# Optimization experiments

Measured on AMD Instinct MI355X. Metric: run time of the kernel, lower is better.

The kernel has to match this reference:

```python
import jax, jax.numpy as jnp
import numpy as np

C_Z, H, C = 128, 4, 32
L = 320
SCALE = 1.0 / np.sqrt(C)
EPS = 1e-5


def setup_inputs() -> dict:
    key = jax.random.key(0)
    ks = jax.random.split(key, 8)
    s = 0.02
    return {
        "z": jax.random.normal(ks[0], (L, L, C_Z), dtype=jnp.float32),
        "pair_mask": jnp.ones((L, L), dtype=jnp.float32),
        "res_mask": jnp.ones((L,), dtype=bool),
        "ln_gamma": jnp.ones((C_Z,), dtype=jnp.float32),
        "ln_beta": jnp.zeros((C_Z,), dtype=jnp.float32),
        "Wq": jax.random.normal(ks[1], (C_Z, H * C), dtype=jnp.float32) * s,
        "Wk": jax.random.normal(ks[2], (C_Z, H * C), dtype=jnp.float32) * s,
        "Wv": jax.random.normal(ks[3], (C_Z, H * C), dtype=jnp.float32) * s,
        "Wb": jax.random.normal(ks[4], (C_Z, H), dtype=jnp.float32) * s,
        "Wg": jax.random.normal(ks[5], (C_Z, H * C), dtype=jnp.float32) * s,
        "Wout": jax.random.normal(ks[6], (H * C, C_Z), dtype=jnp.float32) * s,
    }


def _layernorm(x, gamma, beta):
    mu = jnp.mean(x, axis=-1, keepdims=True)
    var = jnp.mean(jnp.square(x - mu), axis=-1, keepdims=True)
    return (x - mu) * jax.lax.rsqrt(var + EPS) * gamma + beta


def reference(z, pair_mask, res_mask, ln_gamma, ln_beta, Wq, Wk, Wv, Wb, Wg, Wout):
    Ldim = z.shape[0]
    z_ln = _layernorm(z, ln_gamma, ln_beta)                      # [L,L,c_z]
    Q = (z_ln @ Wq).reshape(Ldim, Ldim, H, C)                    # [i,j,h,c]
    K = (z_ln @ Wk).reshape(Ldim, Ldim, H, C)                    # [i,k,h,c]
    V = (z_ln @ Wv).reshape(Ldim, Ldim, H, C)                    # [i,k,h,c]
    B = z_ln @ Wb                                                # [j,k,h]
    G = jax.nn.sigmoid(z_ln @ Wg).reshape(Ldim, Ldim, H, C)      # [i,j,h,c]

    # logits[i,h,j,k] = <Q[i,j], K[i,k]> * scale + B[j,k,h]
    logits = jnp.einsum("ijhc,ikhc->ihjk", Q, K) * SCALE
    logits = logits + jnp.transpose(B, (2, 0, 1))[None]          # +[1,h,j,k]
    neg_inf = jnp.asarray(-jnp.inf, logits.dtype)
    logits = jnp.where(res_mask[None, None, None, :], logits, neg_inf)
    attn = jax.nn.softmax(logits, axis=-1)                       # over k

    out = jnp.einsum("ihjk,ikhc->ijhc", attn, V)                 # [i,j,h,c]
    out = (G * out).reshape(Ldim, Ldim, H * C)
    dz = out @ Wout                                              # [L,L,c_z]
    return dz * pair_mask[..., None]
```

## Files before the change

kernel.cpp:

```cpp
#include <hip/hip_runtime.h>

#define LDIM 320
#define CZ 128
#define NH 4
#define CH 32
#define SCALE2F (0.17677669529663687f * 1.4426950408889634f)
#define LOG2E 1.4426950408889634f
#define LN_EPS 1e-5f

typedef __attribute__((ext_vector_type(8))) short bf16x8;
typedef __attribute__((ext_vector_type(4))) float f32x4;

__device__ __forceinline__ unsigned int pack_bf2(float a, float b) {
  unsigned int ua = __float_as_uint(a);
  unsigned int ub = __float_as_uint(b);
  unsigned int ra = (ua + 0x7fffu + ((ua >> 16) & 1u)) >> 16;
  unsigned int rb = (ub + 0x7fffu + ((ub >> 16) & 1u)) >> 16;
  return (ra & 0xffffu) | (rb << 16);
}

__device__ __forceinline__ unsigned short f2bf(float a) {
  unsigned int ua = __float_as_uint(a);
  return (unsigned short)((ua + 0x7fffu + ((ua >> 16) & 1u)) >> 16);
}

__device__ __forceinline__ float bf2f(unsigned short u) {
  return __uint_as_float(((unsigned int)u) << 16);
}

__global__ __launch_bounds__(256) void k_prep(
    const float* __restrict__ Wq, const float* __restrict__ Wk,
    const float* __restrict__ Wv, const float* __restrict__ Wb,
    const float* __restrict__ Wg, const float* __restrict__ Wout,
    unsigned short* __restrict__ Wt, unsigned short* __restrict__ Woutt)
{
  __shared__ __attribute__((aligned(16))) unsigned short buf[64 * 136];
  const int t = threadIdx.x, bid = blockIdx.x;
  const bool isOut = (bid >= 9);
  const int n0 = isOut ? (bid - 9) * 64 : bid * 64;
  const int nl = t & 63;
  const int n = n0 + nl;
#pragma unroll 8
  for (int it = 0; it < 32; ++it) {
    const int k = (t >> 6) + 4 * it;
    float v;
    if (isOut)        v = Wout[k * 128 + n];
    else if (n < 128) v = Wq[k * 128 + n];
    else if (n < 256) v = Wk[k * 128 + n - 128];
    else if (n < 384) v = Wv[k * 128 + n - 256];
    else if (n < 512) v = Wg[k * 128 + n - 384];
    else if (n < 516) v = Wb[k * 4 + n - 512];
    else              v = 0.f;
    buf[nl * 136 + k] = f2bf(v);
  }
  __syncthreads();
  unsigned short* dst = isOut ? Woutt : Wt;
#pragma unroll
  for (int it = 0; it < 4; ++it) {
    const int idx = t + 256 * it;
    const int rr = idx >> 4, ck = idx & 15;
    const uint4 d = *(const uint4*)&buf[rr * 136 + ck * 8];
    *(uint4*)(dst + (size_t)(n0 + rr) * 128 + ck * 8) = d;
  }
}

__global__ __launch_bounds__(256) void k_lnproj(
    const float* __restrict__ z, const float* __restrict__ gamma,
    const float* __restrict__ beta, const unsigned short* __restrict__ Wt,
    const int* __restrict__ rmask,
    unsigned short* __restrict__ Qg, unsigned short* __restrict__ Kg,
    unsigned short* __restrict__ Vg, unsigned short* __restrict__ Gg,
    float* __restrict__ Bh)
{
  __shared__ __attribute__((aligned(16))) unsigned short As[128 * 136];
  const int t = threadIdx.x;
  const int m0 = blockIdx.x * 128;
  const int rlane = t & 7;

  const float* gp = gamma + rlane * 16;
  const float* bp = beta + rlane * 16;
  const float4 g0 = *(const float4*)(gp + 0);
  const float4 g1 = *(const float4*)(gp + 4);
  const float4 g2 = *(const float4*)(gp + 8);
  const float4 g3 = *(const float4*)(gp + 12);
  const float4 b0 = *(const float4*)(bp + 0);
  const float4 b1 = *(const float4*)(bp + 4);
  const float4 b2 = *(const float4*)(bp + 8);
  const float4 b3 = *(const float4*)(bp + 12);

#pragma unroll
  for (int rr = 0; rr < 4; ++rr) {
    const int row = rr * 32 + (t >> 3);
    const float* zp = z + (size_t)(m0 + row) * CZ + rlane * 16;
    const float4 x0 = *(const float4*)(zp + 0);
    const float4 x1 = *(const float4*)(zp + 4);
    const float4 x2 = *(const float4*)(zp + 8);
    const float4 x3 = *(const float4*)(zp + 12);
    float s  = x0.x + x0.y + x0.z + x0.w + x1.x + x1.y + x1.z + x1.w +
               x2.x + x2.y + x2.z + x2.w + x3.x + x3.y + x3.z + x3.w;
    float ss = x0.x*x0.x + x0.y*x0.y + x0.z*x0.z + x0.w*x0.w +
               x1.x*x1.x + x1.y*x1.y + x1.z*x1.z + x1.w*x1.w +
               x2.x*x2.x + x2.y*x2.y + x2.z*x2.z + x2.w*x2.w +
               x3.x*x3.x + x3.y*x3.y + x3.z*x3.z + x3.w*x3.w;
    s  += __shfl_xor(s, 1);  ss += __shfl_xor(ss, 1);
    s  += __shfl_xor(s, 2);  ss += __shfl_xor(ss, 2);
    s  += __shfl_xor(s, 4);  ss += __shfl_xor(ss, 4);
    const float mu  = s * (1.f / 128.f);
    const float var = ss * (1.f / 128.f) - mu * mu;
    const float rs  = rsqrtf(var + LN_EPS);
    uint4 u0, u1;
    u0.x = pack_bf2((x0.x - mu) * rs * g0.x + b0.x, (x0.y - mu) * rs * g0.y + b0.y);
    u0.y = pack_bf2((x0.z - mu) * rs * g0.z + b0.z, (x0.w - mu) * rs * g0.w + b0.w);
    u0.z = pack_bf2((x1.x - mu) * rs * g1.x + b1.x, (x1.y - mu) * rs * g1.y + b1.y);
    u0.w = pack_bf2((x1.z - mu) * rs * g1.z + b1.z, (x1.w - mu) * rs * g1.w + b1.w);
    u1.x = pack_bf2((x2.x - mu) * rs * g2.x + b2.x, (x2.y - mu) * rs * g2.y + b2.y);
    u1.y = pack_bf2((x2.z - mu) * rs * g2.z + b2.z, (x2.w - mu) * rs * g2.w + b2.w);
    u1.z = pack_bf2((x3.x - mu) * rs * g3.x + b3.x, (x3.y - mu) * rs * g3.y + b3.y);
    u1.w = pack_bf2((x3.z - mu) * rs * g3.z + b3.z, (x3.w - mu) * rs * g3.w + b3.w);
    unsigned short* dst = &As[row * 136 + rlane * 16];
    *(uint4*)(dst + 0) = u0;
    *(uint4*)(dst + 8) = u1;
  }
  __syncthreads();

  const int w = t >> 6, lane = t & 63;
  const int m16 = lane & 15, qd = lane >> 4;
  const f32x4 z4 = {0.f, 0.f, 0.f, 0.f};

  bf16x8 af[2][4];
#pragma unroll
  for (int ks = 0; ks < 4; ++ks) {
    af[0][ks] = *(const bf16x8*)&As[(w * 32 + m16) * 136 + ks * 32 + qd * 8];
    af[1][ks] = *(const bf16x8*)&As[(w * 32 + 16 + m16) * 136 + ks * 32 + qd * 8];
  }

  for (int ntile = 0; ntile < 8; ++ntile) {
    f32x4 acc[2][4];
#pragma unroll
    for (int sub = 0; sub < 2; ++sub)
#pragma unroll
      for (int nt = 0; nt < 4; ++nt) acc[sub][nt] = z4;
#pragma unroll
    for (int ks = 0; ks < 4; ++ks) {
#pragma unroll
      for (int nt = 0; nt < 4; ++nt) {
        const bf16x8 bf = *(const bf16x8*)(
            Wt + (size_t)(ntile * 64 + nt * 16 + m16) * 128 + ks * 32 + qd * 8);
        acc[0][nt] = __builtin_amdgcn_mfma_f32_16x16x32_bf16(af[0][ks], bf, acc[0][nt], 0, 0, 0);
        acc[1][nt] = __builtin_amdgcn_mfma_f32_16x16x32_bf16(af[1][ks], bf, acc[1][nt], 0, 0, 0);
      }
    }
#pragma unroll
    for (int sub = 0; sub < 2; ++sub) {
#pragma unroll
      for (int r = 0; r < 4; ++r) {
        const int p = m0 + w * 32 + sub * 16 + qd * 4 + r;
        const int a = p / 320, bb = p - a * 320;
#pragma unroll
        for (int nt = 0; nt < 4; ++nt) {
          const int n = ntile * 64 + nt * 16 + m16;
          const int off = n & 127, hh = off >> 5, cc = off & 31;
          float val = acc[sub][nt][r];
          if (ntile >= 6) val = 1.f / (1.f + __expf(-val));
          unsigned short* dst =
              (ntile < 2 ? Qg : (ntile < 4 ? Kg : (ntile < 6 ? Vg : Gg)));
          dst[((size_t)(a * 4 + hh) * 320 + bb) * 32 + cc] = f2bf(val);
        }
      }
    }
  }

  {
    f32x4 acc0 = z4, acc1 = z4;
#pragma unroll
    for (int ks = 0; ks < 4; ++ks) {
      const bf16x8 bf = *(const bf16x8*)(
          Wt + (size_t)(512 + m16) * 128 + ks * 32 + qd * 8);
      acc0 = __builtin_amdgcn_mfma_f32_16x16x32_bf16(af[0][ks], bf, acc0, 0, 0, 0);
      acc1 = __builtin_amdgcn_mfma_f32_16x16x32_bf16(af[1][ks], bf, acc1, 0, 0, 0);
    }
    if (m16 < 4) {
#pragma unroll
      for (int r = 0; r < 4; ++r) {
        const int p0 = m0 + w * 32 + qd * 4 + r;
        const int p1 = p0 + 16;
        const float mk0 = rmask[p0 % 320] ? 0.f : -INFINITY;
        const float mk1 = rmask[p1 % 320] ? 0.f : -INFINITY;
        Bh[(size_t)m16 * 102400 + p0] = acc0[r] * LOG2E + mk0;
        Bh[(size_t)m16 * 102400 + p1] = acc1[r] * LOG2E + mk1;
      }
    }
  }
}

__global__ __launch_bounds__(256) void k_attn(
    const unsigned short* __restrict__ Qg, const unsigned short* __restrict__ Kg,
    const unsigned short* __restrict__ Vg, const unsigned short* __restrict__ Gg,
    const float* __restrict__ Bh, unsigned short* __restrict__ Obg)
{
  __shared__ __attribute__((aligned(16))) unsigned short Vt[32 * 328];
  __shared__ __attribute__((aligned(16))) unsigned short Ps[4][16 * 168];
  const int h = blockIdx.x, i = blockIdx.y;
  const int t = threadIdx.x;
  const size_t base = (size_t)(i * NH + h) * (LDIM * CH);

  {
    const int k0 = t >> 3, c4 = (t & 7) * 4;
#pragma unroll
    for (int it = 0; it < 10; ++it) {
      const int k = k0 + 32 * it;
      const uint2 d = *(const uint2*)(Vg + base + k * 32 + c4);
      Vt[(c4 + 0) * 328 + k] = (unsigned short)(d.x & 0xffffu);
      Vt[(c4 + 1) * 328 + k] = (unsigned short)(d.x >> 16);
      Vt[(c4 + 2) * 328 + k] = (unsigned short)(d.y & 0xffffu);
      Vt[(c4 + 3) * 328 + k] = (unsigned short)(d.y >> 16);
    }
  }
  __syncthreads();

  const int w = t >> 6, lane = t & 63;
  const int m16 = lane & 15, qd = lane >> 4;
  const f32x4 z4 = {0.f, 0.f, 0.f, 0.f};

  for (int jt = w; jt < 20; jt += 4) {
    const bf16x8 qfrag =
        *(const bf16x8*)(Qg + base + (size_t)(jt * 16 + m16) * 32 + qd * 8);

    f32x4 acc[20];
    __builtin_amdgcn_s_setprio(1);
#pragma unroll
    for (int kt = 0; kt < 20; ++kt) {
      const bf16x8 kf =
          *(const bf16x8*)(Kg + base + (size_t)(kt * 16 + m16) * 32 + qd * 8);
      acc[kt] = __builtin_amdgcn_mfma_f32_16x16x32_bf16(qfrag, kf, z4, 0, 0, 0);
    }
    __builtin_amdgcn_s_setprio(0);

    const float* bp = Bh + (size_t)h * 102400 +
                      (size_t)(jt * 16 + qd * 4) * 320 + m16;
    float mx[4] = {-INFINITY, -INFINITY, -INFINITY, -INFINITY};
#pragma unroll
    for (int kt = 0; kt < 20; ++kt) {
#pragma unroll
      for (int r = 0; r < 4; ++r) {
        const float s = fmaf(acc[kt][r], SCALE2F, bp[r * 320 + kt * 16]);
        acc[kt][r] = s;
        mx[r] = fmaxf(mx[r], s);
      }
    }
#pragma unroll
    for (int r = 0; r < 4; ++r) {
      mx[r] = fmaxf(mx[r], __shfl_xor(mx[r], 1));
      mx[r] = fmaxf(mx[r], __shfl_xor(mx[r], 2));
      mx[r] = fmaxf(mx[r], __shfl_xor(mx[r], 4));
      mx[r] = fmaxf(mx[r], __shfl_xor(mx[r], 8));
    }
    float l[4] = {0.f, 0.f, 0.f, 0.f};
#pragma unroll
    for (int kt = 0; kt < 20; ++kt) {
#pragma unroll
      for (int r = 0; r < 4; ++r) {
        const float p = __builtin_amdgcn_exp2f(acc[kt][r] - mx[r]);
        acc[kt][r] = p;
        l[r] += p;
      }
    }
#pragma unroll
    for (int r = 0; r < 4; ++r) {
      l[r] += __shfl_xor(l[r], 1);
      l[r] += __shfl_xor(l[r], 2);
      l[r] += __shfl_xor(l[r], 4);
      l[r] += __shfl_xor(l[r], 8);
    }
    float rl[4];
#pragma unroll
    for (int r = 0; r < 4; ++r) rl[r] = __builtin_amdgcn_rcpf(l[r]);

    f32x4 accO0 = z4, accO1 = z4;
#pragma unroll
    for (int hh = 0; hh < 2; ++hh) {
#pragma unroll
      for (int kt2 = 0; kt2 < 10; ++kt2) {
        const int kt = hh * 10 + kt2;
#pragma unroll
        for (int r = 0; r < 4; ++r)
          Ps[w][(qd * 4 + r) * 168 + kt2 * 16 + m16] = f2bf(acc[kt][r]);
      }
      __builtin_amdgcn_s_setprio(1);
#pragma unroll
      for (int ks = 0; ks < 5; ++ks) {
        const bf16x8 pf = *(const bf16x8*)&Ps[w][m16 * 168 + ks * 32 + qd * 8];
        const bf16x8 v0 =
            *(const bf16x8*)&Vt[m16 * 328 + hh * 160 + ks * 32 + qd * 8];
        const bf16x8 v1 =
            *(const bf16x8*)&Vt[(16 + m16) * 328 + hh * 160 + ks * 32 + qd * 8];
        accO0 = __builtin_amdgcn_mfma_f32_16x16x32_bf16(pf, v0, accO0, 0, 0, 0);
        accO1 = __builtin_amdgcn_mfma_f32_16x16x32_bf16(pf, v1, accO1, 0, 0, 0);
      }
      __builtin_amdgcn_s_setprio(0);
    }

#pragma unroll
    for (int r = 0; r < 4; ++r) {
      const int j = jt * 16 + qd * 4 + r;
      const float g0 = bf2f(Gg[base + (size_t)j * 32 + m16]);
      const float g1 = bf2f(Gg[base + (size_t)j * 32 + 16 + m16]);
      unsigned short* op = Obg + (size_t)(i * 320 + j) * 128 + h * 32;
      op[m16]      = f2bf(g0 * rl[r] * accO0[r]);
      op[16 + m16] = f2bf(g1 * rl[r] * accO1[r]);
    }
  }
}

__global__ __launch_bounds__(256) void k_out(
    const unsigned short* __restrict__ Obg, const unsigned short* __restrict__ Woutt,
    const float* __restrict__ pm, float* __restrict__ out)
{
  __shared__ __attribute__((aligned(16))) unsigned short As[128 * 136];
  __shared__ __attribute__((aligned(16))) unsigned short Bs[64 * 136];
  const int t = threadIdx.x;
  const int ntile = blockIdx.x;
  const int m0 = blockIdx.y * 128;

#pragma unroll
  for (int it = 0; it < 8; ++it) {
    const int idx = t + 256 * it;
    const int rr = idx >> 4, ck = idx & 15;
    const uint4 d = *(const uint4*)(Obg + (size_t)(m0 + rr) * 128 + ck * 8);
    *(uint4*)&As[rr * 136 + ck * 8] = d;
  }
  {
    const unsigned short* wrow = Woutt + (size_t)ntile * 64 * 128;
#pragma unroll
    for (int it = 0; it < 4; ++it) {
      const int idx = t + 256 * it;
      const int n = idx >> 4, ck = idx & 15;
      const uint4 d = *(const uint4*)(wrow + n * 128 + ck * 8);
      *(uint4*)&Bs[n * 136 + ck * 8] = d;
    }
  }
  __syncthreads();

  const int w = t >> 6, lane = t & 63;
  const int m16 = lane & 15, qd = lane >> 4;
  const f32x4 z4 = {0.f, 0.f, 0.f, 0.f};
  f32x4 acc[2][4];
#pragma unroll
  for (int sub = 0; sub < 2; ++sub)
#pragma unroll
    for (int nt = 0; nt < 4; ++nt) acc[sub][nt] = z4;

#pragma unroll
  for (int ks = 0; ks < 4; ++ks) {
    const bf16x8 af0 = *(const bf16x8*)&As[(w * 32 + m16) * 136 + qd * 8 + ks * 32];
    const bf16x8 af1 = *(const bf16x8*)&As[(w * 32 + 16 + m16) * 136 + qd * 8 + ks * 32];
#pragma unroll
    for (int nt = 0; nt < 4; ++nt) {
      const bf16x8 bf = *(const bf16x8*)&Bs[(nt * 16 + m16) * 136 + qd * 8 + ks * 32];
      acc[0][nt] = __builtin_amdgcn_mfma_f32_16x16x32_bf16(af0, bf, acc[0][nt], 0, 0, 0);
      acc[1][nt] = __builtin_amdgcn_mfma_f32_16x16x32_bf16(af1, bf, acc[1][nt], 0, 0, 0);
    }
  }

#pragma unroll
  for (int sub = 0; sub < 2; ++sub) {
#pragma unroll
    for (int r = 0; r < 4; ++r) {
      const int p = m0 + w * 32 + sub * 16 + qd * 4 + r;
      const float m = pm[p];
      float* orow = out + (size_t)p * 128 + ntile * 64;
#pragma unroll
      for (int nt = 0; nt < 4; ++nt)
        orow[nt * 16 + m16] = acc[sub][nt][r] * m;
    }
  }
}

extern "C" void kernel_launch(void* const* d_in, const int* in_sizes, int n_in,
                              void* d_out, int out_size, void* d_ws, size_t ws_size,
                              hipStream_t stream)
{
  const float* z     = (const float*)d_in[0];
  const float* pmask = (const float*)d_in[1];
  const int*   rmask = (const int*)d_in[2];
  const float* gamma = (const float*)d_in[3];
  const float* beta  = (const float*)d_in[4];
  const float* Wq    = (const float*)d_in[5];
  const float* Wk    = (const float*)d_in[6];
  const float* Wv    = (const float*)d_in[7];
  const float* Wb    = (const float*)d_in[8];
  const float* Wg    = (const float*)d_in[9];
  const float* Wout  = (const float*)d_in[10];

  const size_t P = (size_t)LDIM * LDIM;
  const size_t E = P * 128;
  char* ws = (char*)d_ws;
  unsigned short* Qg = (unsigned short*)ws;
  unsigned short* Kg = Qg + E;
  unsigned short* Vg = Kg + E;
  unsigned short* Gg = Vg + E;
  unsigned short* Obg = Gg + E;
  unsigned short* Wt = Obg + E;
  unsigned short* Woutt = Wt + 576 * 128;
  float* Bh = (float*)(Woutt + 128 * 128);

  k_prep<<<dim3(11), 256, 0, stream>>>(Wq, Wk, Wv, Wb, Wg, Wout, Wt, Woutt);
  k_lnproj<<<dim3(800), 256, 0, stream>>>(z, gamma, beta, Wt, rmask,
                                          Qg, Kg, Vg, Gg, Bh);
  k_attn<<<dim3(NH, LDIM), 256, 0, stream>>>(Qg, Kg, Vg, Gg, Bh, Obg);
  k_out<<<dim3(2, 800), 256, 0, stream>>>(Obg, Woutt, pmask, (float*)d_out);
}
```

Baseline: 348.5 us.

## Transpose QK^T MFMA to keep P in registers and vectorize projection stores

In the attention kernel, the QK^T MFMA operands are swapped so each lane holds a row of logits. This lets the bias be read as float4, cuts the softmax reductions to two cross-lane shuffles, and builds the P fragment for the PV MFMA in registers with cvt_pk_bf16 and permlane32_swap instead of a round trip through LDS. The projection kernel permutes the weight rows so each lane gets four consecutive output channels, then writes them with one 8-byte packed store instead of four scalar bf16 stores. The trade is more permute and shuffle instructions plus inline asm that is specific to gfx950.

```diff
diff --git a/kernel.cpp b/kernel.cpp
--- a/kernel.cpp
+++ b/kernel.cpp
@@ -26,6 +26,16 @@
 
 __device__ __forceinline__ float bf2f(unsigned short u) {
   return __uint_as_float(((unsigned int)u) << 16);
+}
+
+__device__ __forceinline__ unsigned cvtpk(float a, float b) {
+  unsigned r;
+  asm("v_cvt_pk_bf16_f32 %0, %1, %2" : "=v"(r) : "v"(a), "v"(b));
+  return r;
+}
+
+__device__ __forceinline__ void plswap(unsigned& a, unsigned& b) {
+  asm volatile("v_permlane32_swap_b32 %0, %1" : "+v"(a), "+v"(b));
 }
 
 __global__ __launch_bounds__(256) void k_prep(
@@ -145,27 +155,33 @@
 #pragma unroll
       for (int nt = 0; nt < 4; ++nt) {
         const bf16x8 bf = *(const bf16x8*)(
-            Wt + (size_t)(ntile * 64 + nt * 16 + m16) * 128 + ks * 32 + qd * 8);
+            Wt + (size_t)(ntile * 64 + m16 * 4 + nt) * 128 + ks * 32 + qd * 8);
         acc[0][nt] = __builtin_amdgcn_mfma_f32_16x16x32_bf16(af[0][ks], bf, acc[0][nt], 0, 0, 0);
         acc[1][nt] = __builtin_amdgcn_mfma_f32_16x16x32_bf16(af[1][ks], bf, acc[1][nt], 0, 0, 0);
       }
     }
+    const int cc0 = (m16 * 4) & 31;
+    const int hh = (ntile & 1) * 2 + (m16 >> 3);
+    unsigned short* dstb =
+        (ntile < 2 ? Qg : (ntile < 4 ? Kg : (ntile < 6 ? Vg : Gg)));
 #pragma unroll
     for (int sub = 0; sub < 2; ++sub) {
 #pragma unroll
       for (int r = 0; r < 4; ++r) {
         const int p = m0 + w * 32 + sub * 16 + qd * 4 + r;
         const int a = p / 320, bb = p - a * 320;
-#pragma unroll
-        for (int nt = 0; nt < 4; ++nt) {
-          const int n = ntile * 64 + nt * 16 + m16;
-          const int off = n & 127, hh = off >> 5, cc = off & 31;
-          float val = acc[sub][nt][r];
-          if (ntile >= 6) val = 1.f / (1.f + __expf(-val));
-          unsigned short* dst =
-              (ntile < 2 ? Qg : (ntile < 4 ? Kg : (ntile < 6 ? Vg : Gg)));
-          dst[((size_t)(a * 4 + hh) * 320 + bb) * 32 + cc] = f2bf(val);
+        float v0 = acc[sub][0][r], v1 = acc[sub][1][r];
+        float v2 = acc[sub][2][r], v3 = acc[sub][3][r];
+        if (ntile >= 6) {
+          v0 = 1.f / (1.f + __expf(-v0));
+          v1 = 1.f / (1.f + __expf(-v1));
+          v2 = 1.f / (1.f + __expf(-v2));
+          v3 = 1.f / (1.f + __expf(-v3));
         }
+        uint2 pk;
+        pk.x = pack_bf2(v0, v1);
+        pk.y = pack_bf2(v2, v3);
+        *(uint2*)(dstb + ((size_t)(a * 4 + hh) * 320 + bb) * 32 + cc0) = pk;
       }
     }
   }
@@ -199,7 +215,6 @@
     const float* __restrict__ Bh, unsigned short* __restrict__ Obg)
 {
   __shared__ __attribute__((aligned(16))) unsigned short Vt[32 * 328];
-  __shared__ __attribute__((aligned(16))) unsigned short Ps[4][16 * 168];
   const int h = blockIdx.x, i = blockIdx.y;
   const int t = threadIdx.x;
   const size_t base = (size_t)(i * NH + h) * (LDIM * CH);
@@ -220,6 +235,7 @@
 
   const int w = t >> 6, lane = t & 63;
   const int m16 = lane & 15, qd = lane >> 4;
+  const int odd = qd & 1;
   const f32x4 z4 = {0.f, 0.f, 0.f, 0.f};
 
   for (int jt = w; jt < 20; jt += 4) {
@@ -232,70 +248,75 @@
     for (int kt = 0; kt < 20; ++kt) {
       const bf16x8 kf =
           *(const bf16x8*)(Kg + base + (size_t)(kt * 16 + m16) * 32 + qd * 8);
-      acc[kt] = __builtin_amdgcn_mfma_f32_16x16x32_bf16(qfrag, kf, z4, 0, 0, 0);
+      acc[kt] = __builtin_amdgcn_mfma_f32_16x16x32_bf16(kf, qfrag, z4, 0, 0, 0);
     }
     __builtin_amdgcn_s_setprio(0);
 
-    const float* bp = Bh + (size_t)h * 102400 +
-                      (size_t)(jt * 16 + qd * 4) * 320 + m16;
-    float mx[4] = {-INFINITY, -INFINITY, -INFINITY, -INFINITY};
+    const float* bq = Bh + (size_t)h * 102400 +
+                      (size_t)(jt * 16 + m16) * 320 + qd * 4;
+    float mxa = -INFINITY, mxb = -INFINITY;
 #pragma unroll
     for (int kt = 0; kt < 20; ++kt) {
-#pragma unroll
-      for (int r = 0; r < 4; ++r) {
-        const float s = fmaf(acc[kt][r], SCALE2F, bp[r * 320 + kt * 16]);
-        acc[kt][r] = s;
-        mx[r] = fmaxf(mx[r], s);
-      }
-    }
-#pragma unroll
-    for (int r = 0; r < 4; ++r) {
-      mx[r] = fmaxf(mx[r], __shfl_xor(mx[r], 1));
-      mx[r] = fmaxf(mx[r], __shfl_xor(mx[r], 2));
-      mx[r] = fmaxf(mx[r], __shfl_xor(mx[r], 4));
-      mx[r] = fmaxf(mx[r], __shfl_xor(mx[r], 8));
-    }
-    float l[4] = {0.f, 0.f, 0.f, 0.f};
+      const float4 bv = *(const float4*)(bq + kt * 16);
+      const float s0 = fmaf(acc[kt][0], SCALE2F, bv.x);
+      const float s1 = fmaf(acc[kt][1], SCALE2F, bv.y);
+      const float s2 = fmaf(acc[kt][2], SCALE2F, bv.z);
+      const float s3 = fmaf(acc[kt][3], SCALE2F, bv.w);
+      acc[kt][0] = s0; acc[kt][1] = s1; acc[kt][2] = s2; acc[kt][3] = s3;
+      mxa = fmaxf(mxa, fmaxf(s0, s1));
+      mxb = fmaxf(mxb, fmaxf(s2, s3));
+    }
+    float mx = fmaxf(mxa, mxb);
+    mx = fmaxf(mx, __shfl_xor(mx, 16));
+    mx = fmaxf(mx, __shfl_xor(mx, 32));
+
+    float l0 = 0.f, l1 = 0.f, l2 = 0.f, l3 = 0.f;
 #pragma unroll
     for (int kt = 0; kt < 20; ++kt) {
-#pragma unroll
-      for (int r = 0; r < 4; ++r) {
-        const float p = __builtin_amdgcn_exp2f(acc[kt][r] - mx[r]);
-        acc[kt][r] = p;
-        l[r] += p;
-      }
-    }
-#pragma unroll
-    for (int r = 0; r < 4; ++r) {
-      l[r] += __shfl_xor(l[r], 1);
-      l[r] += __shfl_xor(l[r], 2);
-      l[r] += __shfl_xor(l[r], 4);
-      l[r] += __shfl_xor(l[r], 8);
-    }
-    float rl[4];
-#pragma unroll
-    for (int r = 0; r < 4; ++r) rl[r] = __builtin_amdgcn_rcpf(l[r]);
+      const float p0 = __builtin_amdgcn_exp2f(acc[kt][0] - mx);
+      const float p1 = __builtin_amdgcn_exp2f(acc[kt][1] - mx);
+      const float p2 = __builtin_amdgcn_exp2f(acc[kt][2] - mx);
+      const float p3 = __builtin_amdgcn_exp2f(acc[kt][3] - mx);
+      acc[kt][0] = p0; acc[kt][1] = p1; acc[kt][2] = p2; acc[kt][3] = p3;
+      l0 += p0; l1 += p1; l2 += p2; l3 += p3;
+    }
+    float l = (l0 + l1) + (l2 + l3);
+    l += __shfl_xor(l, 16);
+    l += __shfl_xor(l, 32);
+    const float rl = __builtin_amdgcn_rcpf(l);
+    float rle[4];
+#pragma unroll
+    for (int r = 0; r < 4; ++r) rle[r] = __shfl(rl, qd * 4 + r);
 
     f32x4 accO0 = z4, accO1 = z4;
 #pragma unroll
     for (int hh = 0; hh < 2; ++hh) {
-#pragma unroll
-      for (int kt2 = 0; kt2 < 10; ++kt2) {
-        const int kt = hh * 10 + kt2;
-#pragma unroll
-        for (int r = 0; r < 4; ++r)
-          Ps[w][(qd * 4 + r) * 168 + kt2 * 16 + m16] = f2bf(acc[kt][r]);
+      unsigned Wl[10], Wh[10];
+#pragma unroll
+      for (int kr = 0; kr < 10; ++kr) {
+        Wl[kr] = cvtpk(acc[hh * 10 + kr][0], acc[hh * 10 + kr][1]);
+        Wh[kr] = cvtpk(acc[hh * 10 + kr][2], acc[hh * 10 + kr][3]);
       }
       __builtin_amdgcn_s_setprio(1);
 #pragma unroll
       for (int ks = 0; ks < 5; ++ks) {
-        const bf16x8 pf = *(const bf16x8*)&Ps[w][m16 * 168 + ks * 32 + qd * 8];
+        unsigned a0 = Wl[2 * ks], b0 = Wl[2 * ks + 1];
+        plswap(a0, b0);
+        const unsigned c0 = __shfl_xor(a0, 16), d0 = __shfl_xor(b0, 16);
+        unsigned a1 = Wh[2 * ks], b1 = Wh[2 * ks + 1];
+        plswap(a1, b1);
+        const unsigned c1 = __shfl_xor(a1, 16), d1 = __shfl_xor(b1, 16);
+        union { unsigned u[4]; bf16x8 v; } fr;
+        fr.u[0] = odd ? d0 : a0;
+        fr.u[1] = odd ? d1 : a1;
+        fr.u[2] = odd ? b0 : c0;
+        fr.u[3] = odd ? b1 : c1;
         const bf16x8 v0 =
             *(const bf16x8*)&Vt[m16 * 328 + hh * 160 + ks * 32 + qd * 8];
         const bf16x8 v1 =
             *(const bf16x8*)&Vt[(16 + m16) * 328 + hh * 160 + ks * 32 + qd * 8];
-        accO0 = __builtin_amdgcn_mfma_f32_16x16x32_bf16(pf, v0, accO0, 0, 0, 0);
-        accO1 = __builtin_amdgcn_mfma_f32_16x16x32_bf16(pf, v1, accO1, 0, 0, 0);
+        accO0 = __builtin_amdgcn_mfma_f32_16x16x32_bf16(fr.v, v0, accO0, 0, 0, 0);
+        accO1 = __builtin_amdgcn_mfma_f32_16x16x32_bf16(fr.v, v1, accO1, 0, 0, 0);
       }
       __builtin_amdgcn_s_setprio(0);
     }
@@ -306,8 +327,8 @@
       const float g0 = bf2f(Gg[base + (size_t)j * 32 + m16]);
       const float g1 = bf2f(Gg[base + (size_t)j * 32 + 16 + m16]);
       unsigned short* op = Obg + (size_t)(i * 320 + j) * 128 + h * 32;
-      op[m16]      = f2bf(g0 * rl[r] * accO0[r]);
-      op[16 + m16] = f2bf(g1 * rl[r] * accO1[r]);
+      op[m16]      = f2bf(g0 * rle[r] * accO0[r]);
+      op[16 + m16] = f2bf(g1 * rle[r] * accO1[r]);
     }
   }
 }
```

Result: slower. 362.5 us (+4.0%).
